# Optimization experiments

Hardware: AMD Instinct MI355X
Metric: run time of the kernel (lower is better)

## Reference

```python
import jax, jax.numpy as jnp
import numpy as np

N_NODES = 100000
N_EDGES = 1600000
N_GRAPHS = 512
NEG_SLOPE = 0.2  # PyG GATConv default


def setup_inputs() -> dict:
    key = jax.random.key(0)
    ks = jax.random.split(key, 12)
    x = jax.random.normal(ks[0], (N_NODES, 75), dtype=jnp.float32)
    edge_index = jax.random.randint(ks[1], (2, N_EDGES), 0, N_NODES, dtype=jnp.int64 if jax.config.jax_enable_x64 else jnp.int32)
    batch = jnp.sort(jax.random.randint(ks[2], (N_NODES,), 0, N_GRAPHS, dtype=jnp.int32))
    s = lambda k, shp, fan: jax.random.normal(k, shp, dtype=jnp.float32) * (1.0 / np.sqrt(fan))
    return {
        "x": x, "edge_index": edge_index, "batch": batch,
        "W1": s(ks[3], (75, 64), 75),           # conv1: heads=8, out=8
        "att_src1": s(ks[4], (8, 8), 8),
        "att_dst1": s(ks[5], (8, 8), 8),
        "bias1": jnp.zeros((64,), jnp.float32),
        "W2": s(ks[6], (64, 128), 64),          # conv2: heads=1, out=128
        "att_src2": s(ks[7], (1, 128), 128),
        "att_dst2": s(ks[8], (1, 128), 128),
        "bias2": jnp.zeros((128,), jnp.float32),
        "Wg": s(ks[9], (128, 1), 128),
        "bg": jnp.zeros((1,), jnp.float32),
    }


def _gat_conv(x, src, dst, W, att_src, att_dst, bias, heads, out_ch):
    # x: [N, F_in]; edges src->dst (self-loops already included)
    n = x.shape[0]
    h = (x @ W).reshape(n, heads, out_ch)            # [N, H, C]
    a_src = (h * att_src).sum(-1)                    # [N, H]
    a_dst = (h * att_dst).sum(-1)                    # [N, H]
    e = a_src[src] + a_dst[dst]                      # [E, H]
    e = jax.nn.leaky_relu(e, NEG_SLOPE)
    # segment softmax over incoming edges of each dst node
    emax = jax.ops.segment_max(e, dst, num_segments=n)      # [N, H]
    ee = jnp.exp(e - emax[dst])
    denom = jax.ops.segment_sum(ee, dst, num_segments=n)    # [N, H]
    alpha = ee / denom[dst]                                  # [E, H]
    msg = h[src] * alpha[:, :, None]                          # [E, H, C]
    out = jax.ops.segment_sum(msg, dst, num_segments=n)      # [N, H, C]
    return out.reshape(n, heads * out_ch) + bias


def reference(x, edge_index, batch, W1, att_src1, att_dst1, bias1,
              W2, att_src2, att_dst2, bias2, Wg, bg):
    n = x.shape[0]
    # PyG GATConv adds self-loops by default
    loops = jnp.arange(n, dtype=edge_index.dtype)
    src = jnp.concatenate([edge_index[0], loops])
    dst = jnp.concatenate([edge_index[1], loops])
    # eval mode: dropout is identity
    x2 = jax.nn.elu(_gat_conv(x, src, dst, W1, att_src1, att_dst1, bias1, heads=8, out_ch=8))
    x4 = _gat_conv(x2, src, dst, W2, att_src2, att_dst2, bias2, heads=1, out_ch=128)
    y = jax.ops.segment_sum(x4, batch, num_segments=N_GRAPHS)  # global_add_pool
    return y @ Wg + bg  # [N_GRAPHS, 1]
```

## Files before the change

kernel.cpp:

```cpp
#include <hip/hip_runtime.h>
#include <hip/hip_bf16.h>
#include <math.h>

#define N_NODES 100000
#define N_EDGES 1600000
#define ET (N_EDGES + N_NODES)
#define N_GRAPHS 512
#define NEG_SLOPE 0.2f
#define G2_BLOCKS 1280

#define BSH 7
#define NDB 128
#define NBUCK ((N_NODES + NDB - 1) / NDB)
#define BCAP 2560
#define ABLK 512
#define CHUNK ((ET + ABLK - 1) / ABLK)
#define F1_OFF (ABLK + 3)
#define PRE_GRID (F1_OFF + 1536)

__device__ __forceinline__ void atomAddF(float* p, float v) { unsafeAtomicAdd(p, v); }
__device__ __forceinline__ float lrelu(float v) { return v >= 0.f ? v : NEG_SLOPE * v; }

__device__ __forceinline__ unsigned short f2bf(float f) {
    unsigned int u = __float_as_uint(f);
    u += 0x7FFFu + ((u >> 16) & 1u);
    return (unsigned short)(u >> 16);
}
__device__ __forceinline__ float bf2f(unsigned short s) { return __uint_as_float(((unsigned int)s) << 16); }
__device__ __forceinline__ float bflo(unsigned int p) { return __uint_as_float(p << 16); }
__device__ __forceinline__ float bfhi(unsigned int p) { return __uint_as_float(p & 0xFFFF0000u); }

__global__ __launch_bounds__(256) void k_pre(
    const int* __restrict__ ei, uint2* __restrict__ gbuf, int* __restrict__ bcur,
    const float* __restrict__ x, const float* __restrict__ W1,
    const float* __restrict__ as1, const float* __restrict__ ad1,
    const float* __restrict__ W2, const float* __restrict__ as2,
    const float* __restrict__ ad2, const float* __restrict__ Wg,
    const float* __restrict__ b2, const float* __restrict__ bg,
    unsigned short* __restrict__ h1p, unsigned short* __restrict__ a1sh,
    float* __restrict__ a1d, float* __restrict__ wv, float* __restrict__ out)
{
    __shared__ __align__(16) char smem[CHUNK * 8 + NBUCK * 16 + 1024];
    const int t = threadIdx.x;
    const int blk = blockIdx.x;

    if (blk >= ABLK && blk < F1_OFF) {
        const int bb = blk - ABLK;
        if (bb == 0) {
            if (t < 192) {
                int c = t & 63, which = t >> 6;
                const float* v = (which == 0) ? Wg : ((which == 1) ? as2 : ad2);
                float s = 0.f;
                #pragma unroll
                for (int k = 0; k < 128; ++k) s += W2[c * 128 + k] * v[k];
                wv[which * 64 + c] = s;
            } else if (t == 192) {
                float s = 0.f;
                #pragma unroll
                for (int k = 0; k < 128; ++k) s += b2[k] * Wg[k];
                wv[192] = s;
            }
        } else {
            int i = (bb - 1) * 256 + t;
            if (i < N_GRAPHS) out[i] = bg[0];
        }
        return;
    }

    if (blk >= F1_OFF) {
        float (*xs)[76] = (float (*)[76])smem;
        const int g = t >> 6;
        const int c = t & 63;
        const int vb = blk - F1_OFF;
        const int fstride = PRE_GRID - F1_OFF;
        for (int nb = vb; nb < N_NODES / 4; nb += fstride) {
            const int n = nb * 4 + g;
            const float* xr = x + (long)n * 75;
            xs[g][c] = xr[c];
            if (c < 11) xs[g][64 + c] = xr[64 + c];
            __syncthreads();
            float h = 0.f;
            #pragma unroll
            for (int k = 0; k < 75; ++k) h += xs[g][k] * W1[k * 64 + c];
            h1p[(long)n * 64 + c] = f2bf(h);
            const int head = c >> 3, lane = c & 7;
            float vs = h * as1[c];
            float vd = h * ad1[c];
            #pragma unroll
            for (int off = 1; off < 8; off <<= 1) {
                vs += __shfl_xor(vs, off, 64);
                vd += __shfl_xor(vd, off, 64);
            }
            if (lane == 0) { a1sh[n * 8 + head] = f2bf(vs); a1d[n * 8 + head] = vd; }
            __syncthreads();
        }
        return;
    }

    uint2* pairs = (uint2*)smem;
    int* hist  = (int*)(smem + CHUNK * 8);
    int* excl  = hist + NBUCK;
    int* gbase = excl + NBUCK;
    int* cnt2  = gbase + NBUCK;
    int* red   = cnt2 + NBUCK;
    const long e0 = (long)blk * CHUNK;
    const int  n  = (int)((e0 + CHUNK <= ET) ? CHUNK : (ET - e0));
    for (int i = t; i < NBUCK; i += 256) { hist[i] = 0; cnt2[i] = 0; }
    __syncthreads();
    for (int i = t; i < n; i += 256) {
        long e = e0 + i;
        int dst = (e < N_EDGES) ? ei[N_EDGES + e] : (int)(e - N_EDGES);
        atomicAdd(&hist[dst >> BSH], 1);
    }
    __syncthreads();
    {
        int lk[4]; int s = 0;
        #pragma unroll
        for (int k = 0; k < 4; ++k) {
            int idx = t * 4 + k;
            int v = (idx < NBUCK) ? hist[idx] : 0;
            lk[k] = s; s += v;
        }
        red[t] = s;
        __syncthreads();
        for (int off = 1; off < 256; off <<= 1) {
            int a = (t >= off) ? red[t - off] : 0;
            __syncthreads();
            red[t] += a;
            __syncthreads();
        }
        int p = red[t] - s;
        #pragma unroll
        for (int k = 0; k < 4; ++k) {
            int idx = t * 4 + k;
            if (idx < NBUCK) excl[idx] = p + lk[k];
        }
    }
    __syncthreads();
    for (int i = t; i < n; i += 256) {
        long e = e0 + i;
        int src, dst;
        if (e < N_EDGES) { src = ei[e]; dst = ei[N_EDGES + e]; }
        else             { src = dst = (int)(e - N_EDGES); }
        int b = dst >> BSH;
        int pos = excl[b] + atomicAdd(&cnt2[b], 1);
        pairs[pos] = make_uint2((unsigned)src, (unsigned)dst);
    }
    __syncthreads();
    for (int b = t; b < NBUCK; b += 256)
        gbase[b] = hist[b] ? atomicAdd(&bcur[b], hist[b]) : 0;
    __syncthreads();
    for (int i = t; i < n; i += 256) {
        uint2 pr = pairs[i];
        int b = (int)(pr.y >> BSH);
        gbuf[(long)b * BCAP + gbase[b] + (i - excl[b])] = pr;
    }
}

__global__ __launch_bounds__(512) void k_gat1(
    const uint2* __restrict__ gbuf, const int* __restrict__ bcur,
    int* __restrict__ rowptr, int* __restrict__ ecol,
    const unsigned short* __restrict__ a1sh, const float* __restrict__ a1d,
    const unsigned short* __restrict__ h1p, const float* __restrict__ bias1,
    const float* __restrict__ wv,
    float2* __restrict__ sg2, float* __restrict__ a2dv)
{
    __shared__ int lds_src[BCAP];
    __shared__ int hist[NDB], excl[NDB + 1], cnt2[NDB];
    __shared__ int red[512];
    const int t = threadIdx.x;
    const int b = blockIdx.x;
    const int d0 = b << BSH;
    const int nloc = (N_NODES - d0 < NDB) ? (N_NODES - d0) : NDB;
    int cntr = bcur[b];
    const int cnt = cntr < BCAP ? cntr : BCAP;

    int partial = 0;
    for (int i = t; i < b; i += 512) partial += bcur[i];
    red[t] = partial;
    __syncthreads();
    for (int off = 256; off > 0; off >>= 1) {
        if (t < off) red[t] += red[t + off];
        __syncthreads();
    }
    const int base = red[0];
    __syncthreads();

    if (t < NDB) { hist[t] = 0; cnt2[t] = 0; }
    __syncthreads();
    const uint2* eb = gbuf + (long)b * BCAP;
    for (int i = t; i < cnt; i += 512) atomicAdd(&hist[(int)eb[i].y - d0], 1);
    __syncthreads();
    {
        int v = (t < NDB) ? hist[t] : 0;
        if (t < NDB) red[t] = v;
        __syncthreads();
        for (int off = 1; off < NDB; off <<= 1) {
            int a = (t < NDB && t >= off) ? red[t - off] : 0;
            __syncthreads();
            if (t < NDB) red[t] += a;
            __syncthreads();
        }
        if (t < nloc) excl[t] = red[t] - v;
        if (t == 0) excl[nloc] = cnt;
    }
    __syncthreads();
    if (t < nloc) rowptr[d0 + t] = base + excl[t];
    if (b == NBUCK - 1 && t == 0) rowptr[N_NODES] = base + cnt;
    for (int i = t; i < cnt; i += 512) {
        uint2 pr = eb[i];
        int dl = (int)pr.y - d0;
        int slot = excl[dl] + atomicAdd(&cnt2[dl], 1);
        lds_src[slot] = (int)pr.x;
    }
    __syncthreads();
    for (int i = t; i < cnt; i += 512) ecol[base + i] = lds_src[i];

    const int l = t & 7;
    const int gid = t >> 3;
    for (int dl = gid; dl < nloc; dl += 64) {
        const int dst = d0 + dl;
        const int beg = excl[dl];
        const int dgl = excl[dl + 1] - beg;
        const float adh = a1d[(long)dst * 8 + l];

        float acc[8] = {0.f,0.f,0.f,0.f,0.f,0.f,0.f,0.f};
        float den = 0.f;

        bool v0 = true, v1 = 1 < dgl, v2 = 2 < dgl;
        int s0 = lds_src[beg];
        int s1 = v1 ? lds_src[beg + 1] : 0;
        int s2 = v2 ? lds_src[beg + 2] : 0;
        unsigned short ab0 = a1sh[(long)s0 * 8 + l];
        unsigned short ab1 = a1sh[(long)s1 * 8 + l];
        unsigned short ab2 = a1sh[(long)s2 * 8 + l];
        uint4 pv0 = *(const uint4*)(h1p + (long)s0 * 64 + l * 8);
        uint4 pv1 = *(const uint4*)(h1p + (long)s1 * 64 + l * 8);
        uint4 pv2 = *(const uint4*)(h1p + (long)s2 * 64 + l * 8);

        for (int j = 0; j < dgl; j += 3) {
            float ee;
            ee = v0 ? __expf(lrelu(bf2f(ab0) + adh)) : 0.f;
            den += ee;
            acc[0] += ee * bflo(pv0.x); acc[1] += ee * bfhi(pv0.x);
            acc[2] += ee * bflo(pv0.y); acc[3] += ee * bfhi(pv0.y);
            acc[4] += ee * bflo(pv0.z); acc[5] += ee * bfhi(pv0.z);
            acc[6] += ee * bflo(pv0.w); acc[7] += ee * bfhi(pv0.w);
            v0 = (j + 3) < dgl;
            int sn = v0 ? lds_src[beg + j + 3] : 0;
            ab0 = a1sh[(long)sn * 8 + l];
            pv0 = *(const uint4*)(h1p + (long)sn * 64 + l * 8);

            ee = v1 ? __expf(lrelu(bf2f(ab1) + adh)) : 0.f;
            den += ee;
            acc[0] += ee * bflo(pv1.x); acc[1] += ee * bfhi(pv1.x);
            acc[2] += ee * bflo(pv1.y); acc[3] += ee * bfhi(pv1.y);
            acc[4] += ee * bflo(pv1.z); acc[5] += ee * bfhi(pv1.z);
            acc[6] += ee * bflo(pv1.w); acc[7] += ee * bfhi(pv1.w);
            v1 = (j + 4) < dgl;
            sn = v1 ? lds_src[beg + j + 4] : 0;
            ab1 = a1sh[(long)sn * 8 + l];
            pv1 = *(const uint4*)(h1p + (long)sn * 64 + l * 8);

            ee = v2 ? __expf(lrelu(bf2f(ab2) + adh)) : 0.f;
            den += ee;
            acc[0] += ee * bflo(pv2.x); acc[1] += ee * bfhi(pv2.x);
            acc[2] += ee * bflo(pv2.y); acc[3] += ee * bfhi(pv2.y);
            acc[4] += ee * bflo(pv2.z); acc[5] += ee * bfhi(pv2.z);
            acc[6] += ee * bflo(pv2.w); acc[7] += ee * bfhi(pv2.w);
            v2 = (j + 5) < dgl;
            sn = v2 ? lds_src[beg + j + 5] : 0;
            ab2 = a1sh[(long)sn * 8 + l];
            pv2 = *(const uint4*)(h1p + (long)sn * 64 + l * 8);
        }

        const float inv = 1.f / den;
        float pg = 0.f, ps = 0.f, pd = 0.f;
        #pragma unroll
        for (int k = 0; k < 8; ++k) {
            float vv = acc[k] * inv + bias1[l * 8 + k];
            vv = vv > 0.f ? vv : (__expf(vv) - 1.f);
            pg += vv * wv[l * 8 + k];
            ps += vv * wv[64 + l * 8 + k];
            pd += vv * wv[128 + l * 8 + k];
        }
        #pragma unroll
        for (int off = 1; off < 8; off <<= 1) {
            pg += __shfl_xor(pg, off, 64);
            ps += __shfl_xor(ps, off, 64);
            pd += __shfl_xor(pd, off, 64);
        }
        if (l == 0) { sg2[dst] = make_float2(ps, pg); a2dv[dst] = pd; }
    }
}

__global__ __launch_bounds__(256) void k_gat2(
    const int* __restrict__ rowptr, const int* __restrict__ ecol,
    const float2* __restrict__ sg2, const float* __restrict__ a2dv,
    const float* __restrict__ wv, const int* __restrict__ batch,
    float* __restrict__ out)
{
    const int sl = threadIdx.x & 15;
    const int sgid = ((blockIdx.x * 256 + threadIdx.x) >> 4);
    const int NS = G2_BLOCKS * 16;
    const int per = (N_NODES + NS - 1) / NS;
    const int n0 = sgid * per;
    const int n1 = min(n0 + per, N_NODES);
    const float bc = wv[192];

    float accg = 0.f;
    int curg = -1;
    for (int n = n0; n < n1; ++n) {
        const int beg = rowptr[n], end = rowptr[n + 1];
        const float adv = a2dv[n];
        float num = 0.f, den = 0.f;
        for (int j = beg + sl; j < end; j += 16) {
            int s = ecol[j];
            float2 v = sg2[s];
            float ee = __expf(lrelu(v.x + adv));
            den += ee;
            num += ee * v.y;
        }
        #pragma unroll
        for (int off = 1; off < 16; off <<= 1) {
            den += __shfl_xor(den, off, 64);
            num += __shfl_xor(num, off, 64);
        }
        if (sl == 0) {
            int gr = batch[n];
            if (gr != curg) {
                if (curg >= 0) atomAddF(out + curg, accg);
                curg = gr; accg = 0.f;
            }
            accg += num / den + bc;
        }
    }
    if (sl == 0 && curg >= 0) atomAddF(out + curg, accg);
}

extern "C" void kernel_launch(void* const* d_in, const int* in_sizes, int n_in,
                              void* d_out, int out_size, void* d_ws, size_t ws_size,
                              hipStream_t stream) {
    (void)in_sizes; (void)n_in; (void)out_size; (void)ws_size;
    const float* x     = (const float*)d_in[0];
    const int*   ei    = (const int*)d_in[1];
    const int*   batch = (const int*)d_in[2];
    const float* W1    = (const float*)d_in[3];
    const float* as1   = (const float*)d_in[4];
    const float* ad1   = (const float*)d_in[5];
    const float* b1    = (const float*)d_in[6];
    const float* W2    = (const float*)d_in[7];
    const float* as2   = (const float*)d_in[8];
    const float* ad2   = (const float*)d_in[9];
    const float* b2    = (const float*)d_in[10];
    const float* Wg    = (const float*)d_in[11];
    const float* bg    = (const float*)d_in[12];
    float* out = (float*)d_out;

    const long N = N_NODES;
    char* p = (char*)d_ws;
    int* rowptr = (int*)p;              p += (N + 4)        * sizeof(int);
    int* bcur   = (int*)p;              p += 1024           * sizeof(int);
    int* ecol   = (int*)p;              p += (long)ET       * sizeof(int);
    uint2* gbuf = (uint2*)p;            p += (long)NBUCK * BCAP * sizeof(uint2);
    unsigned short* h1p  = (unsigned short*)p; p += N * 64  * sizeof(unsigned short);
    unsigned short* a1sh = (unsigned short*)p; p += N * 8   * sizeof(unsigned short);
    float* a1d  = (float*)p;            p += N * 8          * sizeof(float);
    float2* sg2 = (float2*)p;           p += N              * sizeof(float2);
    float* a2dv = (float*)p;            p += N              * sizeof(float);
    float* wv   = (float*)p;            p += 256            * sizeof(float);

    hipMemsetAsync(bcur, 0, NBUCK * sizeof(int), stream);
    k_pre <<<PRE_GRID, 256, 0, stream>>>(ei, gbuf, bcur, x, W1, as1, ad1,
                                         W2, as2, ad2, Wg, b2, bg,
                                         h1p, a1sh, a1d, wv, out);
    k_gat1<<<NBUCK, 512, 0, stream>>>(gbuf, bcur, rowptr, ecol,
                                      a1sh, a1d, h1p, b1, wv, sg2, a2dv);
    k_gat2<<<G2_BLOCKS, 256, 0, stream>>>(rowptr, ecol, sg2, a2dv, wv, batch, out);
}
```

Before: 259.4 us.

## Pack edge pairs into 32-bit words, deepen gather pipeline, narrow gat2 subgroups

Packs each bucketed edge into one 32-bit word: the local destination offset goes in the upper bits and the 17-bit source id in the lower bits. This halves the traffic to the global bucket buffer and to shared memory. The scatter to gbuf now has each thread copy one whole bucket serially instead of a strided per-element write, which may hurt coalescing. k_gat1's software-pipelined gather goes from 3 to 5 in-flight edges through macros, raising memory-level parallelism at the cost of registers. k_gat2 uses 8-lane subgroups instead of 16 and assigns twice as many subgroups, which suits the average degree of about 17.

```diff
diff --git a/kernel.cpp b/kernel.cpp
--- a/kernel.cpp
+++ b/kernel.cpp
@@ -17,6 +17,9 @@
 #define CHUNK ((ET + ABLK - 1) / ABLK)
 #define F1_OFF (ABLK + 3)
 #define PRE_GRID (F1_OFF + 1536)
+#define SRC_MASK 131071u
+
+#define BINA_SMEM (CHUNK * 4 + NBUCK * 4 * 4 + 4 + 1024)
 
 __device__ __forceinline__ void atomAddF(float* p, float v) { unsafeAtomicAdd(p, v); }
 __device__ __forceinline__ float lrelu(float v) { return v >= 0.f ? v : NEG_SLOPE * v; }
@@ -31,7 +34,7 @@
 __device__ __forceinline__ float bfhi(unsigned int p) { return __uint_as_float(p & 0xFFFF0000u); }
 
 __global__ __launch_bounds__(256) void k_pre(
-    const int* __restrict__ ei, uint2* __restrict__ gbuf, int* __restrict__ bcur,
+    const int* __restrict__ ei, unsigned* __restrict__ gbuf, int* __restrict__ bcur,
     const float* __restrict__ x, const float* __restrict__ W1,
     const float* __restrict__ as1, const float* __restrict__ ad1,
     const float* __restrict__ W2, const float* __restrict__ as2,
@@ -40,7 +43,7 @@
     unsigned short* __restrict__ h1p, unsigned short* __restrict__ a1sh,
     float* __restrict__ a1d, float* __restrict__ wv, float* __restrict__ out)
 {
-    __shared__ __align__(16) char smem[CHUNK * 8 + NBUCK * 16 + 1024];
+    __shared__ __align__(16) char smem[BINA_SMEM];
     const int t = threadIdx.x;
     const int blk = blockIdx.x;
 
@@ -97,10 +100,10 @@
         return;
     }
 
-    uint2* pairs = (uint2*)smem;
-    int* hist  = (int*)(smem + CHUNK * 8);
+    unsigned* pairs = (unsigned*)smem;
+    int* hist  = (int*)(smem + CHUNK * 4);
     int* excl  = hist + NBUCK;
-    int* gbase = excl + NBUCK;
+    int* gbase = excl + NBUCK + 1;
     int* cnt2  = gbase + NBUCK;
     int* red   = cnt2 + NBUCK;
     const long e0 = (long)blk * CHUNK;
@@ -136,6 +139,7 @@
             if (idx < NBUCK) excl[idx] = p + lk[k];
         }
     }
+    if (t == 0) excl[NBUCK] = n;
     __syncthreads();
     for (int i = t; i < n; i += 256) {
         long e = e0 + i;
@@ -144,21 +148,40 @@
         else             { src = dst = (int)(e - N_EDGES); }
         int b = dst >> BSH;
         int pos = excl[b] + atomicAdd(&cnt2[b], 1);
-        pairs[pos] = make_uint2((unsigned)src, (unsigned)dst);
+        pairs[pos] = ((unsigned)(dst & (NDB - 1)) << 17) | (unsigned)src;
     }
     __syncthreads();
     for (int b = t; b < NBUCK; b += 256)
         gbase[b] = hist[b] ? atomicAdd(&bcur[b], hist[b]) : 0;
     __syncthreads();
-    for (int i = t; i < n; i += 256) {
-        uint2 pr = pairs[i];
-        int b = (int)(pr.y >> BSH);
-        gbuf[(long)b * BCAP + gbase[b] + (i - excl[b])] = pr;
-    }
-}
+    for (int b = t; b < NBUCK; b += 256) {
+        const int s = excl[b], e2 = excl[b + 1];
+        if (s == e2) continue;
+        unsigned* gp = gbuf + (long)b * BCAP + gbase[b];
+        for (int i = s; i < e2; ++i) gp[i - s] = pairs[i];
+    }
+}
+
+#define SLOT_INIT(k) \
+    bool v##k = (k < dgl); \
+    int s##k = v##k ? lds_src[beg + k] : 0; \
+    unsigned short ab##k = a1sh[(long)s##k * 8 + l]; \
+    uint4 pv##k = *(const uint4*)(h1p + (long)s##k * 64 + l * 8);
+
+#define SLOT_STEP(k) { \
+    float ee = v##k ? __expf(lrelu(bf2f(ab##k) + adh)) : 0.f; \
+    den += ee; \
+    acc[0] += ee * bflo(pv##k.x); acc[1] += ee * bfhi(pv##k.x); \
+    acc[2] += ee * bflo(pv##k.y); acc[3] += ee * bfhi(pv##k.y); \
+    acc[4] += ee * bflo(pv##k.z); acc[5] += ee * bfhi(pv##k.z); \
+    acc[6] += ee * bflo(pv##k.w); acc[7] += ee * bfhi(pv##k.w); \
+    v##k = (j + 5 + k) < dgl; \
+    int sn = v##k ? lds_src[beg + j + 5 + k] : 0; \
+    ab##k = a1sh[(long)sn * 8 + l]; \
+    pv##k = *(const uint4*)(h1p + (long)sn * 64 + l * 8); }
 
 __global__ __launch_bounds__(512) void k_gat1(
-    const uint2* __restrict__ gbuf, const int* __restrict__ bcur,
+    const unsigned* __restrict__ gbuf, const int* __restrict__ bcur,
     int* __restrict__ rowptr, int* __restrict__ ecol,
     const unsigned short* __restrict__ a1sh, const float* __restrict__ a1d,
     const unsigned short* __restrict__ h1p, const float* __restrict__ bias1,
@@ -188,8 +211,8 @@
 
     if (t < NDB) { hist[t] = 0; cnt2[t] = 0; }
     __syncthreads();
-    const uint2* eb = gbuf + (long)b * BCAP;
-    for (int i = t; i < cnt; i += 512) atomicAdd(&hist[(int)eb[i].y - d0], 1);
+    const unsigned* eb = gbuf + (long)b * BCAP;
+    for (int i = t; i < cnt; i += 512) atomicAdd(&hist[eb[i] >> 17], 1);
     __syncthreads();
     {
         int v = (t < NDB) ? hist[t] : 0;
@@ -208,10 +231,10 @@
     if (t < nloc) rowptr[d0 + t] = base + excl[t];
     if (b == NBUCK - 1 && t == 0) rowptr[N_NODES] = base + cnt;
     for (int i = t; i < cnt; i += 512) {
-        uint2 pr = eb[i];
-        int dl = (int)pr.y - d0;
+        unsigned pr = eb[i];
+        int dl = (int)(pr >> 17);
         int slot = excl[dl] + atomicAdd(&cnt2[dl], 1);
-        lds_src[slot] = (int)pr.x;
+        lds_src[slot] = (int)(pr & SRC_MASK);
     }
     __syncthreads();
     for (int i = t; i < cnt; i += 512) ecol[base + i] = lds_src[i];
@@ -227,51 +250,10 @@
         float acc[8] = {0.f,0.f,0.f,0.f,0.f,0.f,0.f,0.f};
         float den = 0.f;
 
-        bool v0 = true, v1 = 1 < dgl, v2 = 2 < dgl;
-        int s0 = lds_src[beg];
-        int s1 = v1 ? lds_src[beg + 1] : 0;
-        int s2 = v2 ? lds_src[beg + 2] : 0;
-        unsigned short ab0 = a1sh[(long)s0 * 8 + l];
-        unsigned short ab1 = a1sh[(long)s1 * 8 + l];
-        unsigned short ab2 = a1sh[(long)s2 * 8 + l];
-        uint4 pv0 = *(const uint4*)(h1p + (long)s0 * 64 + l * 8);
-        uint4 pv1 = *(const uint4*)(h1p + (long)s1 * 64 + l * 8);
-        uint4 pv2 = *(const uint4*)(h1p + (long)s2 * 64 + l * 8);
-
-        for (int j = 0; j < dgl; j += 3) {
-            float ee;
-            ee = v0 ? __expf(lrelu(bf2f(ab0) + adh)) : 0.f;
-            den += ee;
-            acc[0] += ee * bflo(pv0.x); acc[1] += ee * bfhi(pv0.x);
-            acc[2] += ee * bflo(pv0.y); acc[3] += ee * bfhi(pv0.y);
-            acc[4] += ee * bflo(pv0.z); acc[5] += ee * bfhi(pv0.z);
-            acc[6] += ee * bflo(pv0.w); acc[7] += ee * bfhi(pv0.w);
-            v0 = (j + 3) < dgl;
-            int sn = v0 ? lds_src[beg + j + 3] : 0;
-            ab0 = a1sh[(long)sn * 8 + l];
-            pv0 = *(const uint4*)(h1p + (long)sn * 64 + l * 8);
-
-            ee = v1 ? __expf(lrelu(bf2f(ab1) + adh)) : 0.f;
-            den += ee;
-            acc[0] += ee * bflo(pv1.x); acc[1] += ee * bfhi(pv1.x);
-            acc[2] += ee * bflo(pv1.y); acc[3] += ee * bfhi(pv1.y);
-            acc[4] += ee * bflo(pv1.z); acc[5] += ee * bfhi(pv1.z);
-            acc[6] += ee * bflo(pv1.w); acc[7] += ee * bfhi(pv1.w);
-            v1 = (j + 4) < dgl;
-            sn = v1 ? lds_src[beg + j + 4] : 0;
-            ab1 = a1sh[(long)sn * 8 + l];
-            pv1 = *(const uint4*)(h1p + (long)sn * 64 + l * 8);
-
-            ee = v2 ? __expf(lrelu(bf2f(ab2) + adh)) : 0.f;
-            den += ee;
-            acc[0] += ee * bflo(pv2.x); acc[1] += ee * bfhi(pv2.x);
-            acc[2] += ee * bflo(pv2.y); acc[3] += ee * bfhi(pv2.y);
-            acc[4] += ee * bflo(pv2.z); acc[5] += ee * bfhi(pv2.z);
-            acc[6] += ee * bflo(pv2.w); acc[7] += ee * bfhi(pv2.w);
-            v2 = (j + 5) < dgl;
-            sn = v2 ? lds_src[beg + j + 5] : 0;
-            ab2 = a1sh[(long)sn * 8 + l];
-            pv2 = *(const uint4*)(h1p + (long)sn * 64 + l * 8);
+        SLOT_INIT(0) SLOT_INIT(1) SLOT_INIT(2) SLOT_INIT(3) SLOT_INIT(4)
+
+        for (int j = 0; j < dgl; j += 5) {
+            SLOT_STEP(0) SLOT_STEP(1) SLOT_STEP(2) SLOT_STEP(3) SLOT_STEP(4)
         }
 
         const float inv = 1.f / den;
@@ -300,9 +282,9 @@
     const float* __restrict__ wv, const int* __restrict__ batch,
     float* __restrict__ out)
 {
-    const int sl = threadIdx.x & 15;
-    const int sgid = ((blockIdx.x * 256 + threadIdx.x) >> 4);
-    const int NS = G2_BLOCKS * 16;
+    const int sl = threadIdx.x & 7;
+    const int sgid = ((blockIdx.x * 256 + threadIdx.x) >> 3);
+    const int NS = G2_BLOCKS * 32;
     const int per = (N_NODES + NS - 1) / NS;
     const int n0 = sgid * per;
     const int n1 = min(n0 + per, N_NODES);
@@ -314,7 +296,7 @@
         const int beg = rowptr[n], end = rowptr[n + 1];
         const float adv = a2dv[n];
         float num = 0.f, den = 0.f;
-        for (int j = beg + sl; j < end; j += 16) {
+        for (int j = beg + sl; j < end; j += 8) {
             int s = ecol[j];
             float2 v = sg2[s];
             float ee = __expf(lrelu(v.x + adv));
@@ -322,7 +304,7 @@
             num += ee * v.y;
         }
         #pragma unroll
-        for (int off = 1; off < 16; off <<= 1) {
+        for (int off = 1; off < 8; off <<= 1) {
             den += __shfl_xor(den, off, 64);
             num += __shfl_xor(num, off, 64);
         }
@@ -362,7 +344,7 @@
     int* rowptr = (int*)p;              p += (N + 4)        * sizeof(int);
     int* bcur   = (int*)p;              p += 1024           * sizeof(int);
     int* ecol   = (int*)p;              p += (long)ET       * sizeof(int);
-    uint2* gbuf = (uint2*)p;            p += (long)NBUCK * BCAP * sizeof(uint2);
+    unsigned* gbuf = (unsigned*)p;      p += (long)NBUCK * BCAP * sizeof(unsigned);
     unsigned short* h1p  = (unsigned short*)p; p += N * 64  * sizeof(unsigned short);
     unsigned short* a1sh = (unsigned short*)p; p += N * 8   * sizeof(unsigned short);
     float* a1d  = (float*)p;            p += N * 8          * sizeof(float);
```

Measured after the change: 265.7 us. 1.02x slower.
